# Optimization experiments

Measured on AMD Instinct MI355X. Metric: run time of the kernel, lower is better.

## Reference

```python
import jax, jax.numpy as jnp
import numpy as np

B, S = 16, 32            # batch, cfg.feature_samples
CF, CC, H, W = 768, 512, 28, 28
NEG = 2                  # cfg.neg_samples
POS_INTRA_SHIFT, POS_INTER_SHIFT, NEG_INTER_SHIFT = 0.18, 0.12, 0.46


def _norm(t):
    # F.normalize(t, dim=1, eps=1e-10)
    n = jnp.sqrt(jnp.sum(t * t, axis=1, keepdims=True))
    return t / jnp.maximum(n, 1e-10)


def _grid_sample(img, grid):
    # torch F.grid_sample, bilinear, padding_mode='border', align_corners=True
    # img [B,C,H,W], grid [B,Hg,Wg,2] with (x,y) in [-1,1]
    Hh, Ww = img.shape[2], img.shape[3]
    x = (grid[..., 0] + 1.0) * 0.5 * (Ww - 1)
    y = (grid[..., 1] + 1.0) * 0.5 * (Hh - 1)
    x0 = jnp.floor(x); y0 = jnp.floor(y)
    wx = x - x0; wy = y - y0
    x0c = jnp.clip(x0, 0, Ww - 1).astype(jnp.int32)
    x1c = jnp.clip(x0 + 1, 0, Ww - 1).astype(jnp.int32)
    y0c = jnp.clip(y0, 0, Hh - 1).astype(jnp.int32)
    y1c = jnp.clip(y0 + 1, 0, Hh - 1).astype(jnp.int32)
    gather = jax.vmap(lambda im, yy, xx: im[:, yy, xx])  # -> [B,C,Hg,Wg]
    Ia, Ib = gather(img, y0c, x0c), gather(img, y1c, x0c)
    Ic, Id = gather(img, y0c, x1c), gather(img, y1c, x1c)
    wx = wx[:, None]; wy = wy[:, None]
    return Ia * (1 - wx) * (1 - wy) + Ib * (1 - wx) * wy + Ic * wx * (1 - wy) + Id * wx * wy


def _sample(t, coords):
    # sample(): grid_sample(t, coords.permute(0,2,1,3))
    return _grid_sample(t, jnp.transpose(coords, (0, 2, 1, 3)))


def _corr(a, b):
    return jnp.einsum('nchw,ncij->nhwij', a, b)


def _helper(f1, f2, c1, c2, shift):
    # fd computed under no_grad in torch
    fd = jax.lax.stop_gradient(_corr(_norm(f1), _norm(f2)))
    # cfg.pointwise = True
    old_mean = fd.mean()
    fd = fd - fd.mean(axis=(3, 4), keepdims=True)
    fd = fd - fd.mean() + old_mean
    cd = _corr(_norm(c1), _norm(c2))
    # cfg.zero_clamp=True, cfg.stabalize=False -> cd.clamp(0.0)
    return -jnp.maximum(cd, 0.0) * (fd - shift)


def setup_inputs() -> dict:
    key = jax.random.key(0)
    ks = jax.random.split(key, 11)
    return {
        'orig_feats': jax.random.normal(ks[0], (B, CF, H, W), jnp.float32),
        'orig_feats_pos': jax.random.normal(ks[1], (B, CF, H, W), jnp.float32),
        'orig_salience': jax.random.uniform(ks[2], (B, 224, 224), jnp.float32),
        'orig_salience_pos': jax.random.uniform(ks[3], (B, 224, 224), jnp.float32),
        'orig_code': jax.random.normal(ks[4], (B, CC, H, W), jnp.float32),
        'orig_code_pos': jax.random.normal(ks[5], (B, CC, H, W), jnp.float32),
        'depth': jax.random.uniform(ks[6], (B, 1, 224, 224), jnp.float32),
        'depth_pos': jax.random.uniform(ks[7], (B, 1, 224, 224), jnp.float32),
        'coords1': jax.random.uniform(ks[8], (B, S, S, 2), jnp.float32),
        'coords2': jax.random.uniform(ks[9], (B, S, S, 2), jnp.float32),
        'perms': jax.random.randint(ks[10], (NEG, B), 0, B, jnp.int32),
    }


def reference(orig_feats, orig_feats_pos, orig_salience, orig_salience_pos,
              orig_code, orig_code_pos, depth, depth_pos,
              coords1, coords2, perms):
    # random-coordinate branch: coords = rand(...) * 2 - 1
    c1 = coords1 * 2.0 - 1.0
    c2 = coords2 * 2.0 - 1.0
    feats = _sample(orig_feats, c1)
    code = _sample(orig_code, c1)
    feats_pos = _sample(orig_feats_pos, c2)
    code_pos = _sample(orig_code_pos, c2)

    pos_intra = _helper(feats, feats, code, code, POS_INTRA_SHIFT).mean()
    pos_inter = _helper(feats, feats_pos, code, code_pos, POS_INTER_SHIFT).mean()

    def neg_one(perm):
        feats_neg = _sample(orig_feats[perm], c2)
        code_neg = _sample(orig_code[perm], c2)
        return _helper(feats, feats_neg, code, code_neg, NEG_INTER_SHIFT).mean()

    neg_inter = jax.vmap(neg_one)(perms).mean()
    return jnp.stack([pos_intra, pos_inter, neg_inter])
```

## Files before the change

### kernel.cpp

```cpp
#include <hip/hip_runtime.h>
#include <hip/hip_bf16.h>

#define NB 16
#define NP 1024
#define CF 768
#define CC 512
#define HH 28
#define WW 28
#define HW 784
#define NTOT 16777216.0f

typedef float f32x4 __attribute__((ext_vector_type(4)));
struct __align__(8) bf4 { __hip_bfloat16 a, b, c, d; };

__device__ __forceinline__ float b2f(__hip_bfloat16 h) { return __bfloat162float(h); }


__global__ void transpose_bf16_kernel(const float* __restrict__ in0,
                                      const float* __restrict__ in1,
                                      __hip_bfloat16* __restrict__ out, int C) {
  __shared__ float tile[32][33];
  int p0 = blockIdx.x * 32, c0 = blockIdx.y * 32;
  int t = blockIdx.z >> 4, b = blockIdx.z & 15;
  int tx = threadIdx.x, ty = threadIdx.y;
  const float* ib = (t == 0 ? in0 : in1) + (size_t)b * C * HW;
  __hip_bfloat16* ob = out + ((size_t)t * NB + b) * HW * C;
#pragma unroll
  for (int i = 0; i < 32; i += 8) {
    int c = c0 + ty + i, p = p0 + tx;
    if (p < HW) tile[ty + i][tx] = ib[(size_t)c * HW + p];
  }
  __syncthreads();
#pragma unroll
  for (int i = 0; i < 32; i += 8) {
    int p = p0 + ty + i, c = c0 + tx;
    if (p < HW) ob[(size_t)p * C + c] = __float2bfloat16(tile[tx][ty + i]);
  }
}

__global__ __launch_bounds__(256) void sample_pack_kernel(
    const __hip_bfloat16* __restrict__ fTb, const __hip_bfloat16* __restrict__ cTb,
    const float* __restrict__ coords1, const float* __restrict__ coords2,
    const int* __restrict__ perms,
    unsigned char* __restrict__ Fb, unsigned char* __restrict__ Cb,
    float* __restrict__ scF, float* __restrict__ scC) {
  __shared__ int offs[4][64];
  __shared__ float wts[4][64];
  __shared__ char tile[4160];

  int bb = blockIdx.y, slot = blockIdx.z;
  int tid = threadIdx.x;
  int p0 = blockIdx.x * 64;
  int pt = blockIdx.x >> 1, mh = blockIdx.x & 1;

  const float* coords = (slot == 0) ? coords1 : coords2;
  int srcidx;
  if (slot == 0)      srcidx = bb;
  else if (slot == 1) srcidx = 16 + bb;
  else if (slot == 2) srcidx = perms[bb];
  else                srcidx = perms[16 + bb];

  if (tid < 64) {
    int p = p0 + tid;
    float cx = coords[((size_t)bb * NP + p) * 2 + 0];
    float cy = coords[((size_t)bb * NP + p) * 2 + 1];
    float x = cx * (WW - 1), y = cy * (HH - 1);
    float x0f = floorf(x), y0f = floorf(y);
    float wx = x - x0f, wy = y - y0f;
    int x0 = min(max((int)x0f, 0), WW - 1);
    int x1 = min(max((int)x0f + 1, 0), WW - 1);
    int y0 = min(max((int)y0f, 0), HH - 1);
    int y1 = min(max((int)y0f + 1, 0), HH - 1);
    offs[0][tid] = y0 * WW + x0;
    offs[1][tid] = y1 * WW + x0;
    offs[2][tid] = y0 * WW + x1;
    offs[3][tid] = y1 * WW + x1;
    wts[0][tid] = (1.f - wx) * (1.f - wy);
    wts[1][tid] = (1.f - wx) * wy;
    wts[2][tid] = wx * (1.f - wy);
    wts[3][tid] = wx * wy;
  }
  __syncthreads();

  int gid = tid >> 4, l = tid & 15;
  int r = l >> 1, h4 = l & 1;

  {
    const __hip_bfloat16* base = fTb + (size_t)srcidx * HW * CF;
    float ssq[4] = {0.f, 0.f, 0.f, 0.f};
    for (int kt = 0; kt < 12; ++kt) {
#pragma unroll
      for (int j = 0; j < 4; ++j) {
        int m = j * 16 + gid;
        float4 v = {0.f, 0.f, 0.f, 0.f};
#pragma unroll
        for (int c = 0; c < 4; ++c) {
          const bf4 t4 = *((const bf4*)(base + (size_t)offs[c][m] * CF) + kt * 16 + l);
          float wv = wts[c][m];
          v.x += wv * b2f(t4.a); v.y += wv * b2f(t4.b);
          v.z += wv * b2f(t4.c); v.w += wv * b2f(t4.d);
        }
        ssq[j] += v.x * v.x + v.y * v.y + v.z * v.z + v.w * v.w;
        int w0 = __builtin_amdgcn_cvt_pk_fp8_f32(v.x, v.y, 0, false);
        int w1 = __builtin_amdgcn_cvt_pk_fp8_f32(v.z, v.w, w0, true);
        *(int*)(tile + r * 520 + m * 8 + h4 * 4) = w1;
      }
      __syncthreads();
      unsigned char* gbase = Fb +
          (((((size_t)slot * NB + bb) * 12 + kt) * 8 + pt) * 1024 + (size_t)mh * 64) * 8;
#pragma unroll
      for (int jj = 0; jj < 2; ++jj) {
        int cl = jj * 256 + tid;
        int rr = cl >> 6, mi = cl & 63;
        unsigned long long val = *(const unsigned long long*)(tile + rr * 520 + mi * 8);
        *(unsigned long long*)(gbase + (size_t)(rr * 128 + mi) * 8) = val;
      }
      __syncthreads();
    }
#pragma unroll
    for (int j = 0; j < 4; ++j) {
#pragma unroll
      for (int mm = 1; mm < 16; mm <<= 1) ssq[j] += __shfl_xor(ssq[j], mm);
    }
    if (l == 0) {
#pragma unroll
      for (int j = 0; j < 4; ++j) {
        int p = p0 + j * 16 + gid;
        scF[((size_t)slot * NB + bb) * NP + p] = 1.f / fmaxf(sqrtf(ssq[j]), 1e-10f);
      }
    }
  }

  {
    const __hip_bfloat16* base = cTb + (size_t)srcidx * HW * CC;
    float ssq[4] = {0.f, 0.f, 0.f, 0.f};
    for (int kt = 0; kt < 8; ++kt) {
#pragma unroll
      for (int j = 0; j < 4; ++j) {
        int m = j * 16 + gid;
        float4 v = {0.f, 0.f, 0.f, 0.f};
#pragma unroll
        for (int c = 0; c < 4; ++c) {
          const bf4 t4 = *((const bf4*)(base + (size_t)offs[c][m] * CC) + kt * 16 + l);
          float wv = wts[c][m];
          v.x += wv * b2f(t4.a); v.y += wv * b2f(t4.b);
          v.z += wv * b2f(t4.c); v.w += wv * b2f(t4.d);
        }
        ssq[j] += v.x * v.x + v.y * v.y + v.z * v.z + v.w * v.w;
        int w0 = __builtin_amdgcn_cvt_pk_fp8_f32(v.x, v.y, 0, false);
        int w1 = __builtin_amdgcn_cvt_pk_fp8_f32(v.z, v.w, w0, true);
        *(int*)(tile + r * 520 + m * 8 + h4 * 4) = w1;
      }
      __syncthreads();
      unsigned char* gbase = Cb +
          (((((size_t)slot * NB + bb) * 8 + kt) * 8 + pt) * 1024 + (size_t)mh * 64) * 8;
#pragma unroll
      for (int jj = 0; jj < 2; ++jj) {
        int cl = jj * 256 + tid;
        int rr = cl >> 6, mi = cl & 63;
        unsigned long long val = *(const unsigned long long*)(tile + rr * 520 + mi * 8);
        *(unsigned long long*)(gbase + (size_t)(rr * 128 + mi) * 8) = val;
      }
      __syncthreads();
    }
#pragma unroll
    for (int j = 0; j < 4; ++j) {
#pragma unroll
      for (int mm = 1; mm < 16; mm <<= 1) ssq[j] += __shfl_xor(ssq[j], mm);
    }
    if (l == 0) {
#pragma unroll
      for (int j = 0; j < 4; ++j) {
        int p = p0 + j * 16 + gid;
        scC[((size_t)slot * NB + bb) * NP + p] = 1.f / fmaxf(sqrtf(ssq[j]), 1e-10f);
      }
    }
  }
}

__device__ __forceinline__ void stage_sup(const unsigned long long* __restrict__ st,
                                          unsigned long long* buf, int tid) {
#pragma unroll
  for (int i = 0; i < 2; ++i) {
    const char* g = (const char*)st + (size_t)(i * 256 + tid) * 16;
    char* d = (char*)buf + i * 4096 + (tid & 192) * 16;
    __builtin_amdgcn_global_load_lds(
        (const __attribute__((address_space(1))) void*)g,
        (__attribute__((address_space(3))) void*)d, 16, 0, 0);
  }
}

__global__ __launch_bounds__(256, 2) void corr_kernel(
    const unsigned long long* __restrict__ Fb,
    const unsigned long long* __restrict__ Cb,
    const float* __restrict__ scF, const float* __restrict__ scC,
    float* __restrict__ rowfd, float* __restrict__ rowrcd,
    float* __restrict__ cross) {
  __shared__ unsigned long long Afs[1024], Bfs[1024], Acs[1024], Bcs[1024];

  int id = blockIdx.x;
  int zl = id & 7, q = id >> 3;
  int bx = q & 7, by = (q >> 3) & 7, zh = q >> 6;
  int z = zh * 8 + zl;
  int h = z >> 4, bb = z & 15;
  int p0 = bx * 128, q0 = by * 128;
  int tid = threadIdx.x, ln = tid & 63, w = tid >> 6;
  int wm = w >> 1, wn = w & 1, quad = ln >> 4, t16 = ln & 15;

  const unsigned long long* AfB = Fb + (((size_t)bb * 12) * 8 + bx) * 1024;
  const unsigned long long* BfB = Fb + ((((size_t)h * NB + bb) * 12) * 8 + by) * 1024;
  const unsigned long long* AcB = Cb + (((size_t)bb * 8) * 8 + bx) * 1024;
  const unsigned long long* BcB = Cb + ((((size_t)h * NB + bb) * 8) * 8 + by) * 1024;
  const size_t KTSTR = (size_t)8 * 1024;

  f32x4 accf[4][4], accc[4][4];
#pragma unroll
  for (int i = 0; i < 4; ++i)
#pragma unroll
    for (int j = 0; j < 4; ++j) {
      accf[i][j] = (f32x4){0.f, 0.f, 0.f, 0.f};
      accc[i][j] = (f32x4){0.f, 0.f, 0.f, 0.f};
    }

  for (int kt = 0; kt < 12; ++kt) {
    stage_sup(AfB + kt * KTSTR, Afs, tid);
    stage_sup(BfB + kt * KTSTR, Bfs, tid);
    if (kt < 8) {
      stage_sup(AcB + kt * KTSTR, Acs, tid);
      stage_sup(BcB + kt * KTSTR, Bcs, tid);
    }
    __syncthreads();
#pragma unroll
    for (int s = 0; s < 2; ++s) {
      long a[4], b[4];
#pragma unroll
      for (int mi = 0; mi < 4; ++mi)
        a[mi] = (long)Afs[s * 512 + quad * 128 + wm * 64 + mi * 16 + t16];
#pragma unroll
      for (int ni = 0; ni < 4; ++ni)
        b[ni] = (long)Bfs[s * 512 + quad * 128 + wn * 64 + ni * 16 + t16];
#pragma unroll
      for (int mi = 0; mi < 4; ++mi)
#pragma unroll
        for (int ni = 0; ni < 4; ++ni)
          accf[mi][ni] = __builtin_amdgcn_mfma_f32_16x16x32_fp8_fp8(
              a[mi], b[ni], accf[mi][ni], 0, 0, 0);
    }
    if (kt < 8) {
#pragma unroll
      for (int s = 0; s < 2; ++s) {
        long a[4], b[4];
#pragma unroll
        for (int mi = 0; mi < 4; ++mi)
          a[mi] = (long)Acs[s * 512 + quad * 128 + wm * 64 + mi * 16 + t16];
#pragma unroll
        for (int ni = 0; ni < 4; ++ni)
          b[ni] = (long)Bcs[s * 512 + quad * 128 + wn * 64 + ni * 16 + t16];
#pragma unroll
        for (int mi = 0; mi < 4; ++mi)
#pragma unroll
          for (int ni = 0; ni < 4; ++ni)
            accc[mi][ni] = __builtin_amdgcn_mfma_f32_16x16x32_fp8_fp8(
                a[mi], b[ni], accc[mi][ni], 0, 0, 0);
      }
    }
    __syncthreads();
  }

  float* sm = (float*)Afs;
  {
    const float* s0 = scF + (size_t)bb * NP;
    const float* s1 = scF + ((size_t)h * NB + bb) * NP;
    const float* s2 = scC + (size_t)bb * NP;
    const float* s3 = scC + ((size_t)h * NB + bb) * NP;
    if (tid < 128) {
      sm[tid] = s0[p0 + tid];
      sm[256 + tid] = s2[p0 + tid];
    } else {
      int u = tid - 128;
      sm[128 + u] = s1[q0 + u];
      sm[384 + u] = s3[q0 + u];
    }
  }
  __syncthreads();

  float sbf[4], sbc[4];
#pragma unroll
  for (int ni = 0; ni < 4; ++ni) {
    int qq = wn * 64 + ni * 16 + t16;
    sbf[ni] = sm[128 + qq];
    sbc[ni] = sm[384 + qq];
  }
  float cross_l = 0.f;
#pragma unroll
  for (int mi = 0; mi < 4; ++mi) {
#pragma unroll
    for (int r = 0; r < 4; ++r) {
      int pl = wm * 64 + mi * 16 + quad * 4 + r;
      float saf = sm[pl], sac = sm[256 + pl];
      float sfd = 0.f, srw = 0.f;
#pragma unroll
      for (int ni = 0; ni < 4; ++ni) {
        float fd = accf[mi][ni][r] * (saf * sbf[ni]);
        float cd = accc[mi][ni][r] * (sac * sbc[ni]);
        float rc = fmaxf(cd, 0.f);
        sfd += fd;
        srw += rc;
        cross_l += rc * fd;
      }
#pragma unroll
      for (int mm = 1; mm < 16; mm <<= 1) {
        sfd += __shfl_xor(sfd, mm);
        srw += __shfl_xor(srw, mm);
      }
      if (t16 == 0) {
        int p = p0 + pl;
        size_t idx = ((size_t)h * NB + bb) * NP + p;
        atomicAdd(&rowfd[idx], sfd);
        atomicAdd(&rowrcd[idx], srw);
      }
    }
  }
#pragma unroll
  for (int mm = 1; mm < 64; mm <<= 1) cross_l += __shfl_xor(cross_l, mm);
  float* crs = (float*)Bfs;
  if (ln == 0) crs[w] = cross_l;
  __syncthreads();
  if (tid == 0) atomicAdd(&cross[h], crs[0] + crs[1] + crs[2] + crs[3]);
}

__global__ void finalize_partial(const float* __restrict__ rowfd,
                                 const float* __restrict__ rowrcd,
                                 const float* __restrict__ cross,
                                 float* __restrict__ losses) {
  __shared__ float r1[16], r2[16], r3[16];
  const float shifts[4] = {0.18f, 0.12f, 0.46f, 0.46f};
  int h = blockIdx.x, tid = threadIdx.x, w = tid >> 6, ln = tid & 63;
  float s1 = 0.f, s2 = 0.f, s3 = 0.f;
  for (int i = tid; i < NB * NP; i += 1024) {
    float a = rowfd[h * NB * NP + i];
    float c = rowrcd[h * NB * NP + i];
    s1 += a;
    s2 += c;
    s3 += a * c;
  }
#pragma unroll
  for (int mm = 1; mm < 64; mm <<= 1) {
    s1 += __shfl_xor(s1, mm);
    s2 += __shfl_xor(s2, mm);
    s3 += __shfl_xor(s3, mm);
  }
  if (ln == 0) { r1[w] = s1; r2[w] = s2; r3[w] = s3; }
  __syncthreads();
  if (tid == 0) {
    float Sfd = 0.f, Srcd = 0.f, Sdot = 0.f;
#pragma unroll
    for (int i = 0; i < 16; ++i) { Sfd += r1[i]; Srcd += r2[i]; Sdot += r3[i]; }
    losses[h] = -(cross[h] - Sdot * (1.0f / 1024.0f) +
                  (Sfd / NTOT - shifts[h]) * Srcd) / NTOT;
  }
}

__global__ void finalize_combine(const float* __restrict__ losses,
                                 float* __restrict__ out) {
  if (threadIdx.x == 0) {
    out[0] = losses[0];
    out[1] = losses[1];
    out[2] = 0.5f * (losses[2] + losses[3]);
  }
}

extern "C" void kernel_launch(void* const* d_in, const int* in_sizes, int n_in,
                              void* d_out, int out_size, void* d_ws, size_t ws_size,
                              hipStream_t stream) {
  (void)in_sizes; (void)n_in; (void)out_size; (void)ws_size;
  const float* orig_feats = (const float*)d_in[0];
  const float* orig_feats_pos = (const float*)d_in[1];
  const float* orig_code = (const float*)d_in[4];
  const float* orig_code_pos = (const float*)d_in[5];
  const float* coords1 = (const float*)d_in[8];
  const float* coords2 = (const float*)d_in[9];
  const int* perms = (const int*)d_in[10];
  float* out = (float*)d_out;

  char* ws = (char*)d_ws;
  size_t off = 0;
  __hip_bfloat16* fTb = (__hip_bfloat16*)(ws + off); off += (size_t)2 * NB * HW * CF * 2;
  __hip_bfloat16* cTb = (__hip_bfloat16*)(ws + off); off += (size_t)2 * NB * HW * CC * 2;
  unsigned char* Fb = (unsigned char*)(ws + off); off += (size_t)4 * NB * NP * CF;
  unsigned char* Cb = (unsigned char*)(ws + off); off += (size_t)4 * NB * NP * CC;
  float* rowfd  = (float*)(ws + off); off += (size_t)4 * NB * NP * 4;
  float* rowrcd = (float*)(ws + off); off += (size_t)4 * NB * NP * 4;
  float* cross  = (float*)(ws + off); off += 64;
  float* losses = (float*)(ws + off); off += 64;
  float* scF    = (float*)(ws + off); off += (size_t)4 * NB * NP * 4;
  float* scC    = (float*)(ws + off); off += (size_t)4 * NB * NP * 4;

  (void)hipMemsetAsync(rowfd, 0, (size_t)4 * NB * NP * 4 * 2 + 128, stream);

  dim3 tb(32, 8);
  transpose_bf16_kernel<<<dim3(25, 24, 32), tb, 0, stream>>>(
      orig_feats, orig_feats_pos, fTb, CF);
  transpose_bf16_kernel<<<dim3(25, 16, 32), tb, 0, stream>>>(
      orig_code, orig_code_pos, cTb, CC);
  sample_pack_kernel<<<dim3(16, 16, 4), 256, 0, stream>>>(
      fTb, cTb, coords1, coords2, perms, Fb, Cb, scF, scC);

  corr_kernel<<<dim3(4096), 256, 0, stream>>>(
      (const unsigned long long*)Fb, (const unsigned long long*)Cb,
      scF, scC, rowfd, rowrcd, cross);
  finalize_partial<<<4, 1024, 0, stream>>>(rowfd, rowrcd, cross, losses);
  finalize_combine<<<1, 64, 0, stream>>>(losses, out);
}
```

Baseline: 416.3 us.

## Double-buffer LDS staging in corr kernel to overlap loads with MFMA

Makes the fp8 correlation GEMM kernel use two LDS buffers for each operand tile. The next k-tile is prefetched with global_load_lds while MFMAs run on the current one, and a vmcnt wait plus a barrier replaces the two per-iteration __syncthreads. The aim is to hide global-memory latency behind compute. In exchange, LDS use doubles from 32KB to 64KB per block, which may lower occupancy below the launch_bounds target of 2 blocks per CU.

Result: no change. 410.7 us (-1.4%).

```diff
diff --git a/kernel.cpp b/kernel.cpp
--- a/kernel.cpp
+++ b/kernel.cpp
@@ -196,7 +196,8 @@
     const float* __restrict__ scF, const float* __restrict__ scC,
     float* __restrict__ rowfd, float* __restrict__ rowrcd,
     float* __restrict__ cross) {
-  __shared__ unsigned long long Afs[1024], Bfs[1024], Acs[1024], Bcs[1024];
+  __shared__ unsigned long long Afs[2][1024], Bfs[2][1024],
+                                Acs[2][1024], Bcs[2][1024];
 
   int id = blockIdx.x;
   int zl = id & 7, q = id >> 3;
@@ -222,23 +223,35 @@
       accc[i][j] = (f32x4){0.f, 0.f, 0.f, 0.f};
     }
 
+  stage_sup(AfB, Afs[0], tid);
+  stage_sup(BfB, Bfs[0], tid);
+  stage_sup(AcB, Acs[0], tid);
+  stage_sup(BcB, Bcs[0], tid);
+  asm volatile("s_waitcnt vmcnt(0)" ::: "memory");
+  __builtin_amdgcn_s_barrier();
+
+  int cur = 0;
   for (int kt = 0; kt < 12; ++kt) {
-    stage_sup(AfB + kt * KTSTR, Afs, tid);
-    stage_sup(BfB + kt * KTSTR, Bfs, tid);
-    if (kt < 8) {
-      stage_sup(AcB + kt * KTSTR, Acs, tid);
-      stage_sup(BcB + kt * KTSTR, Bcs, tid);
-    }
-    __syncthreads();
+    int nxt = cur ^ 1;
+    if (kt + 1 < 12) {
+      stage_sup(AfB + (kt + 1) * KTSTR, Afs[nxt], tid);
+      stage_sup(BfB + (kt + 1) * KTSTR, Bfs[nxt], tid);
+      if (kt + 1 < 8) {
+        stage_sup(AcB + (kt + 1) * KTSTR, Acs[nxt], tid);
+        stage_sup(BcB + (kt + 1) * KTSTR, Bcs[nxt], tid);
+      }
+    }
+    const unsigned long long* Af = Afs[cur];
+    const unsigned long long* Bf = Bfs[cur];
 #pragma unroll
     for (int s = 0; s < 2; ++s) {
       long a[4], b[4];
 #pragma unroll
       for (int mi = 0; mi < 4; ++mi)
-        a[mi] = (long)Afs[s * 512 + quad * 128 + wm * 64 + mi * 16 + t16];
+        a[mi] = (long)Af[s * 512 + quad * 128 + wm * 64 + mi * 16 + t16];
 #pragma unroll
       for (int ni = 0; ni < 4; ++ni)
-        b[ni] = (long)Bfs[s * 512 + quad * 128 + wn * 64 + ni * 16 + t16];
+        b[ni] = (long)Bf[s * 512 + quad * 128 + wn * 64 + ni * 16 + t16];
 #pragma unroll
       for (int mi = 0; mi < 4; ++mi)
 #pragma unroll
@@ -247,15 +260,17 @@
               a[mi], b[ni], accf[mi][ni], 0, 0, 0);
     }
     if (kt < 8) {
+      const unsigned long long* Ac = Acs[cur];
+      const unsigned long long* Bc = Bcs[cur];
 #pragma unroll
       for (int s = 0; s < 2; ++s) {
         long a[4], b[4];
 #pragma unroll
         for (int mi = 0; mi < 4; ++mi)
-          a[mi] = (long)Acs[s * 512 + quad * 128 + wm * 64 + mi * 16 + t16];
+          a[mi] = (long)Ac[s * 512 + quad * 128 + wm * 64 + mi * 16 + t16];
 #pragma unroll
         for (int ni = 0; ni < 4; ++ni)
-          b[ni] = (long)Bcs[s * 512 + quad * 128 + wn * 64 + ni * 16 + t16];
+          b[ni] = (long)Bc[s * 512 + quad * 128 + wn * 64 + ni * 16 + t16];
 #pragma unroll
         for (int mi = 0; mi < 4; ++mi)
 #pragma unroll
@@ -264,7 +279,9 @@
                 a[mi], b[ni], accc[mi][ni], 0, 0, 0);
       }
     }
-    __syncthreads();
+    asm volatile("s_waitcnt vmcnt(0)" ::: "memory");
+    __builtin_amdgcn_s_barrier();
+    cur = nxt;
   }
 
   float* sm = (float*)Afs;
```

## Double-buffer LDS staging in corr_kernel with manual vmcnt waits and barriers

Applied to the files above, without the earlier changes.

Double-buffers the shared-memory tiles of the feature and code correlation GEMMs, so global-to-LDS loads for the next K step are issued before the MFMA work on the current step. The old per-iteration `__syncthreads` pairs are replaced by explicit `s_waitcnt vmcnt` counts and raw barriers. `s_setprio` is raised around the MFMA blocks. LDS use per block doubles, and the hand-tuned wait counts and barrier placement are fragile. In the late feature-only iterations a buffer may be refilled while slower waves are still reading it.

New measurement: 414.6 us. About the same (-0.4%).

```diff
diff --git a/kernel.cpp b/kernel.cpp
--- a/kernel.cpp
+++ b/kernel.cpp
@@ -190,13 +190,37 @@
   }
 }
 
+__device__ __forceinline__ void mfma_tile(const unsigned long long* __restrict__ A,
+                                          const unsigned long long* __restrict__ B,
+                                          int aoff, int boff, f32x4 acc[4][4]) {
+#pragma unroll
+  for (int s = 0; s < 2; ++s) {
+    long a[4], b[4];
+#pragma unroll
+    for (int mi = 0; mi < 4; ++mi) a[mi] = (long)A[s * 512 + aoff + mi * 16];
+#pragma unroll
+    for (int ni = 0; ni < 4; ++ni) b[ni] = (long)B[s * 512 + boff + ni * 16];
+#pragma unroll
+    for (int mi = 0; mi < 4; ++mi)
+#pragma unroll
+      for (int ni = 0; ni < 4; ++ni)
+        acc[mi][ni] = __builtin_amdgcn_mfma_f32_16x16x32_fp8_fp8(
+            a[mi], b[ni], acc[mi][ni], 0, 0, 0);
+  }
+}
+
+#define WAITV(N) asm volatile("s_waitcnt vmcnt(" #N ")" ::: "memory")
+#define BAR() do { __builtin_amdgcn_s_barrier(); \
+                   __builtin_amdgcn_sched_barrier(0); } while (0)
+
 __global__ __launch_bounds__(256, 2) void corr_kernel(
     const unsigned long long* __restrict__ Fb,
     const unsigned long long* __restrict__ Cb,
     const float* __restrict__ scF, const float* __restrict__ scC,
     float* __restrict__ rowfd, float* __restrict__ rowrcd,
     float* __restrict__ cross) {
-  __shared__ unsigned long long Afs[1024], Bfs[1024], Acs[1024], Bcs[1024];
+  __shared__ unsigned long long Afs[2][1024], Bfs[2][1024],
+                                Acs[2][1024], Bcs[2][1024];
 
   int id = blockIdx.x;
   int zl = id & 7, q = id >> 3;
@@ -206,6 +230,8 @@
   int p0 = bx * 128, q0 = by * 128;
   int tid = threadIdx.x, ln = tid & 63, w = tid >> 6;
   int wm = w >> 1, wn = w & 1, quad = ln >> 4, t16 = ln & 15;
+  int aoff = quad * 128 + wm * 64 + t16;
+  int boff = quad * 128 + wn * 64 + t16;
 
   const unsigned long long* AfB = Fb + (((size_t)bb * 12) * 8 + bx) * 1024;
   const unsigned long long* BfB = Fb + ((((size_t)h * NB + bb) * 12) * 8 + by) * 1024;
@@ -222,49 +248,38 @@
       accc[i][j] = (f32x4){0.f, 0.f, 0.f, 0.f};
     }
 
+  stage_sup(AfB, Afs[0], tid);
+  stage_sup(BfB, Bfs[0], tid);
+  stage_sup(AcB, Acs[0], tid);
+  stage_sup(BcB, Bcs[0], tid);
+  stage_sup(AfB + KTSTR, Afs[1], tid);
+  stage_sup(BfB + KTSTR, Bfs[1], tid);
+
+#pragma unroll
   for (int kt = 0; kt < 12; ++kt) {
-    stage_sup(AfB + kt * KTSTR, Afs, tid);
-    stage_sup(BfB + kt * KTSTR, Bfs, tid);
+    const int cur = kt & 1, nxt = cur ^ 1;
+    if (kt >= 1 && kt < 11) {
+      stage_sup(AfB + (size_t)(kt + 1) * KTSTR, Afs[nxt], tid);
+      stage_sup(BfB + (size_t)(kt + 1) * KTSTR, Bfs[nxt], tid);
+    }
+    if (kt <= 7)       { WAITV(8); }
+    else if (kt <= 10) { WAITV(4); }
+    else               { WAITV(0); }
+    BAR();
+    __builtin_amdgcn_s_setprio(1);
+    mfma_tile(Afs[cur], Bfs[cur], aoff, boff, accf);
+    __builtin_amdgcn_s_setprio(0);
     if (kt < 8) {
-      stage_sup(AcB + kt * KTSTR, Acs, tid);
-      stage_sup(BcB + kt * KTSTR, Bcs, tid);
-    }
-    __syncthreads();
-#pragma unroll
-    for (int s = 0; s < 2; ++s) {
-      long a[4], b[4];
-#pragma unroll
-      for (int mi = 0; mi < 4; ++mi)
-        a[mi] = (long)Afs[s * 512 + quad * 128 + wm * 64 + mi * 16 + t16];
-#pragma unroll
-      for (int ni = 0; ni < 4; ++ni)
-        b[ni] = (long)Bfs[s * 512 + quad * 128 + wn * 64 + ni * 16 + t16];
-#pragma unroll
-      for (int mi = 0; mi < 4; ++mi)
-#pragma unroll
-        for (int ni = 0; ni < 4; ++ni)
-          accf[mi][ni] = __builtin_amdgcn_mfma_f32_16x16x32_fp8_fp8(
-              a[mi], b[ni], accf[mi][ni], 0, 0, 0);
-    }
-    if (kt < 8) {
-#pragma unroll
-      for (int s = 0; s < 2; ++s) {
-        long a[4], b[4];
-#pragma unroll
-        for (int mi = 0; mi < 4; ++mi)
-          a[mi] = (long)Acs[s * 512 + quad * 128 + wm * 64 + mi * 16 + t16];
-#pragma unroll
-        for (int ni = 0; ni < 4; ++ni)
-          b[ni] = (long)Bcs[s * 512 + quad * 128 + wn * 64 + ni * 16 + t16];
-#pragma unroll
-        for (int mi = 0; mi < 4; ++mi)
-#pragma unroll
-          for (int ni = 0; ni < 4; ++ni)
-            accc[mi][ni] = __builtin_amdgcn_mfma_f32_16x16x32_fp8_fp8(
-                a[mi], b[ni], accc[mi][ni], 0, 0, 0);
-      }
-    }
-    __syncthreads();
+      if (kt < 7) {
+        stage_sup(AcB + (size_t)(kt + 1) * KTSTR, Acs[nxt], tid);
+        stage_sup(BcB + (size_t)(kt + 1) * KTSTR, Bcs[nxt], tid);
+      }
+      if (kt <= 6) { WAITV(8); } else { WAITV(4); }
+      BAR();
+      __builtin_amdgcn_s_setprio(1);
+      mfma_tile(Acs[cur], Bcs[cur], aoff, boff, accc);
+      __builtin_amdgcn_s_setprio(0);
+    }
   }
 
   float* sm = (float*)Afs;
```
